# Kernel optimization log

Measured on AMD Instinct MI355X. Metric: run time of the kernel, lower is better.

The kernel has to match this reference:

```python
import jax, jax.numpy as jnp
import numpy as np

B, T, C = 2, 1024, 768
H, NE, K = 3072, 8, 2


def setup_inputs() -> dict:
    key = jax.random.key(0)
    k1, k2, k3, k4 = jax.random.split(key, 4)
    x = jax.random.normal(k1, (B, T, C), dtype=jnp.float32)
    w_fc = jax.random.normal(k2, (C, H * NE), dtype=jnp.float32) * 0.02
    w_proj = jax.random.normal(k3, (H * NE, C), dtype=jnp.float32) * (0.02 * (2 * 12) ** -0.5)
    w_gate = jax.random.normal(k4, (C, NE), dtype=jnp.float32) * 0.02
    return {"x": x, "w_fc": w_fc, "w_proj": w_proj, "w_gate": w_gate}


def reference(x, w_fc, w_proj, w_gate):
    # Router: softmax over experts, top-k, renormalize selected probs.
    router_logits = jnp.einsum('btc,ce->bte', x, w_gate)
    router_probs = jax.nn.softmax(router_logits, axis=-1)
    top_p, top_i = jax.lax.top_k(router_probs, K)          # (B,T,K)
    top_p = top_p / jnp.sum(top_p, axis=-1, keepdims=True)

    # First projection. Original gathers (C,H,B,T,K) weight slices then
    # einsum('btc,chbtk->bthk'); mathematically identical to projecting with
    # all experts and gathering the selected outputs (same contraction order).
    wf = w_fc.reshape(C, H, NE)
    h_all = jnp.einsum('btc,che->bthe', x, wf)             # (B,T,H,NE)
    h = jnp.take_along_axis(h_all, top_i[:, :, None, :], axis=-1)  # (B,T,H,K)
    h = jax.nn.gelu(h, approximate=True)

    # Second projection + weighted combine over the K selected experts.
    wp = w_proj.reshape(H, C, NE)
    o_all = jnp.einsum('bthk,hce->btcke', h, wp)           # (B,T,C,K,NE)
    o = jnp.take_along_axis(o_all, top_i[:, :, None, :, None], axis=-1)[..., 0]  # (B,T,C,K)
    o = jnp.einsum('btck,btk->btc', o, top_p)
    return o
```

## Files before the change

kernel.cpp:

```cpp
#include <hip/hip_runtime.h>
#include <hip/hip_bf16.h>
#include <math.h>

#define BB 2
#define TT 1024
#define CC 768
#define HH 3072
#define NEXP 8
#define NTOK (BB*TT)
#define CAP 1024
#define CNT_STRIDE 32

typedef __attribute__((ext_vector_type(8))) short short8;
typedef __attribute__((ext_vector_type(4))) float float4v;

typedef const __attribute__((address_space(1))) void* gptr_t;
typedef __attribute__((address_space(3))) void* sptr_t;

__device__ __forceinline__ unsigned short f2bf(float f) {
    unsigned int u = __float_as_uint(f);
    unsigned int r = (u + 0x7fffu + ((u >> 16) & 1u)) >> 16;
    return (unsigned short)r;
}
__device__ __forceinline__ float gelu_tanh(float v) {
    const float k2 = 2.0f * 0.7978845608028654f;
    const float k1 = 0.044715f;
    float z = k2 * (v + k1 * v * v * v);
    return v / (1.0f + __expf(-z));
}

__global__ void router_kernel(const float* __restrict__ x,
                              const float* __restrict__ w_gate,
                              float* __restrict__ top_p,
                              int* __restrict__ counts,
                              int* __restrict__ tok_list) {
    int t = blockIdx.x;
    int lane = threadIdx.x;
    float acc[NEXP];
#pragma unroll
    for (int e = 0; e < NEXP; ++e) acc[e] = 0.f;
    for (int c = lane; c < CC; c += 64) {
        float xv = x[t * CC + c];
        const float4* wg = (const float4*)(w_gate + c * NEXP);
        float4 w0 = wg[0], w1 = wg[1];
        acc[0] += xv * w0.x; acc[1] += xv * w0.y;
        acc[2] += xv * w0.z; acc[3] += xv * w0.w;
        acc[4] += xv * w1.x; acc[5] += xv * w1.y;
        acc[6] += xv * w1.z; acc[7] += xv * w1.w;
    }
#pragma unroll
    for (int e = 0; e < NEXP; ++e) {
        for (int off = 32; off > 0; off >>= 1)
            acc[e] += __shfl_down(acc[e], off, 64);
    }
    if (lane == 0) {
        float m = acc[0];
#pragma unroll
        for (int e = 1; e < NEXP; ++e) m = fmaxf(m, acc[e]);
        float p[NEXP]; float s = 0.f;
#pragma unroll
        for (int e = 0; e < NEXP; ++e) { p[e] = expf(acc[e] - m); s += p[e]; }
        float inv_s = 1.f / s;
#pragma unroll
        for (int e = 0; e < NEXP; ++e) p[e] *= inv_s;
        int i0 = 0;
#pragma unroll
        for (int e = 1; e < NEXP; ++e) if (p[e] > p[i0]) i0 = e;
        int i1 = (i0 == 0) ? 1 : 0;
#pragma unroll
        for (int e = 0; e < NEXP; ++e) if (e != i0 && p[e] > p[i1]) i1 = e;
        float p0 = p[i0], p1 = p[i1];
        float inv = 1.f / (p0 + p1);
        top_p[t * 2 + 0] = p0 * inv;
        top_p[t * 2 + 1] = p1 * inv;
        int pos0 = atomicAdd(&counts[i0 * CNT_STRIDE], 1);
        if (pos0 < CAP) tok_list[i0 * NTOK + pos0] = t * 2 + 0;
        int pos1 = atomicAdd(&counts[i1 * CNT_STRIDE], 1);
        if (pos1 < CAP) tok_list[i1 * NTOK + pos1] = t * 2 + 1;
    }
}

__global__ __launch_bounds__(256)
void permute_w(const float* __restrict__ In, unsigned short* __restrict__ Out,
               int Adim, int Bdim) {
    __shared__ unsigned short L[128 * 66];
    int a0 = blockIdx.x * 128;
    int b0 = blockIdx.y * 8;
    int t = threadIdx.x;
#pragma unroll
    for (int j = 0; j < 8; ++j) {
        int idx = j * 256 + t;
        int r = idx >> 4, c4 = idx & 15;
        const float4 v = *(const float4*)(In + (size_t)(a0 + r) * Bdim * 8 + b0 * 8 + c4 * 4);
        ushort2 s01, s23;
        s01.x = f2bf(v.x); s01.y = f2bf(v.y);
        s23.x = f2bf(v.z); s23.y = f2bf(v.w);
        *(ushort2*)&L[r * 66 + c4 * 4]     = s01;
        *(ushort2*)&L[r * 66 + c4 * 4 + 2] = s23;
    }
    __syncthreads();
    int w = t >> 6, ln = t & 63;
    int oc = w * 16 + (ln & 15);
    int e = oc & 7, b = b0 + (oc >> 3);
    unsigned short* dst = Out + ((size_t)e * Bdim + b) * Adim + a0;
#pragma unroll
    for (int p = 0; p < 4; ++p) {
        int seg = (ln >> 4) + p * 4;
        short8 vv;
#pragma unroll
        for (int k = 0; k < 8; ++k) vv[k] = (short)L[(seg * 8 + k) * 66 + oc];
        *(short8*)(dst + seg * 8) = vv;
    }
}

__global__ void gather_x(const float* __restrict__ x,
                         const int* __restrict__ counts,
                         const int* __restrict__ tok_list,
                         unsigned short* __restrict__ xg) {
    int pos = blockIdx.x;
    int e = pos >> 10, i = pos & (CAP - 1);
    int M = counts[e * CNT_STRIDE]; if (M > CAP) M = CAP;
    int Mr = (M + 127) & ~127; if (Mr > CAP) Mr = CAP;
    if (i >= Mr) return;
    int c = threadIdx.x * 4;
    unsigned short* dst = xg + (size_t)pos * CC + c;
    ushort4 s;
    if (i < M) {
        int tk = tok_list[e * NTOK + i] >> 1;
        float4 v = *(const float4*)(x + (size_t)tk * CC + c);
        s.x = f2bf(v.x); s.y = f2bf(v.y); s.z = f2bf(v.z); s.w = f2bf(v.w);
    } else {
        s.x = s.y = s.z = s.w = 0;
    }
    *(ushort4*)dst = s;
}

__global__ __launch_bounds__(256)
void gemm1_mfma(const unsigned short* __restrict__ xg,
                const unsigned short* __restrict__ wfc_b,
                const int* __restrict__ counts,
                unsigned short* __restrict__ h_slab) {
    int e = blockIdx.z;
    int M = counts[e * CNT_STRIDE]; if (M > CAP) M = CAP;
    int m0 = blockIdx.y * 128;
    if (m0 >= M) return;
    int n0 = blockIdx.x * 128;

    __shared__ unsigned short As[2][128 * 32];
    __shared__ unsigned short Bs[2][128 * 32];

    int tid = threadIdx.x;
    int wave = tid >> 6, lane = tid & 63;
    int wm = wave >> 1, wn = wave & 1;
    int quad = lane >> 4, l16 = lane & 15;

    const unsigned short* aBase = xg + ((size_t)e * CAP + m0) * CC;
    const unsigned short* bBase = wfc_b + ((size_t)e * HH + n0) * CC;

    int srow = wave * 32 + (lane >> 2);
    int schunk = (lane & 3) * 8;

    float4v acc[4][4];
#pragma unroll
    for (int i = 0; i < 4; ++i)
#pragma unroll
        for (int j = 0; j < 4; ++j)
#pragma unroll
            for (int r = 0; r < 4; ++r) acc[i][j][r] = 0.f;

#pragma unroll
    for (int q = 0; q < 2; ++q) {
        int r = srow + q * 16;
        __builtin_amdgcn_global_load_lds(
            (gptr_t)(aBase + (size_t)r * CC + schunk),
            (sptr_t)(&As[0][(wave * 32 + q * 16) * 32]), 16, 0, 0);
        __builtin_amdgcn_global_load_lds(
            (gptr_t)(bBase + (size_t)r * CC + schunk),
            (sptr_t)(&Bs[0][(wave * 32 + q * 16) * 32]), 16, 0, 0);
    }

    for (int k0 = 0; k0 < CC; k0 += 32) {
        int cur = (k0 >> 5) & 1;
        __syncthreads();
        if (k0 + 32 < CC) {
            int nxt = cur ^ 1;
#pragma unroll
            for (int q = 0; q < 2; ++q) {
                int r = srow + q * 16;
                __builtin_amdgcn_global_load_lds(
                    (gptr_t)(aBase + (size_t)r * CC + k0 + 32 + schunk),
                    (sptr_t)(&As[nxt][(wave * 32 + q * 16) * 32]), 16, 0, 0);
                __builtin_amdgcn_global_load_lds(
                    (gptr_t)(bBase + (size_t)r * CC + k0 + 32 + schunk),
                    (sptr_t)(&Bs[nxt][(wave * 32 + q * 16) * 32]), 16, 0, 0);
            }
        }
        short8 af[4], bf[4];
#pragma unroll
        for (int mt = 0; mt < 4; ++mt)
            af[mt] = *(const short8*)&As[cur][(wm * 64 + mt * 16 + l16) * 32 + quad * 8];
#pragma unroll
        for (int nt = 0; nt < 4; ++nt)
            bf[nt] = *(const short8*)&Bs[cur][(wn * 64 + nt * 16 + l16) * 32 + quad * 8];
#pragma unroll
        for (int mt = 0; mt < 4; ++mt)
#pragma unroll
            for (int nt = 0; nt < 4; ++nt)
                acc[mt][nt] = __builtin_amdgcn_mfma_f32_16x16x32_bf16(
                    af[mt], bf[nt], acc[mt][nt], 0, 0, 0);
    }

#pragma unroll
    for (int mt = 0; mt < 4; ++mt) {
#pragma unroll
        for (int r = 0; r < 4; ++r) {
            int m = m0 + wm * 64 + mt * 16 + quad * 4 + r;
            unsigned short* orow = h_slab + ((size_t)e * CAP + m) * HH + n0 + wn * 64 + l16;
#pragma unroll
            for (int nt = 0; nt < 4; ++nt)
                orow[nt * 16] = f2bf(gelu_tanh(acc[mt][nt][r]));
        }
    }
}

__global__ __launch_bounds__(256)
void gemm2_mfma(const unsigned short* __restrict__ h_slab,
                const unsigned short* __restrict__ wp_b,
                const int* __restrict__ counts,
                const int* __restrict__ tok_list,
                float* __restrict__ o_part) {
    int e = blockIdx.z;
    int M = counts[e * CNT_STRIDE]; if (M > CAP) M = CAP;
    int m0 = blockIdx.y * 128;
    if (m0 >= M) return;
    int n0 = (blockIdx.x >> 2) * 128;
    int ks = blockIdx.x & 3;

    __shared__ unsigned short As[2][128 * 32];
    __shared__ unsigned short Bs[2][128 * 32];

    int tid = threadIdx.x;
    int wave = tid >> 6, lane = tid & 63;
    int wm = wave >> 1, wn = wave & 1;
    int quad = lane >> 4, l16 = lane & 15;

    const unsigned short* aBase = h_slab + ((size_t)e * CAP + m0) * HH + ks * 768;
    const unsigned short* bBase = wp_b + ((size_t)e * CC + n0) * HH + ks * 768;

    int srow = wave * 32 + (lane >> 2);
    int schunk = (lane & 3) * 8;

    float4v acc[4][4];
#pragma unroll
    for (int i = 0; i < 4; ++i)
#pragma unroll
        for (int j = 0; j < 4; ++j)
#pragma unroll
            for (int r = 0; r < 4; ++r) acc[i][j][r] = 0.f;

#pragma unroll
    for (int q = 0; q < 2; ++q) {
        int r = srow + q * 16;
        __builtin_amdgcn_global_load_lds(
            (gptr_t)(aBase + (size_t)r * HH + schunk),
            (sptr_t)(&As[0][(wave * 32 + q * 16) * 32]), 16, 0, 0);
        __builtin_amdgcn_global_load_lds(
            (gptr_t)(bBase + (size_t)r * HH + schunk),
            (sptr_t)(&Bs[0][(wave * 32 + q * 16) * 32]), 16, 0, 0);
    }

    for (int k0 = 0; k0 < 768; k0 += 32) {
        int cur = (k0 >> 5) & 1;
        __syncthreads();
        if (k0 + 32 < 768) {
            int nxt = cur ^ 1;
#pragma unroll
            for (int q = 0; q < 2; ++q) {
                int r = srow + q * 16;
                __builtin_amdgcn_global_load_lds(
                    (gptr_t)(aBase + (size_t)r * HH + k0 + 32 + schunk),
                    (sptr_t)(&As[nxt][(wave * 32 + q * 16) * 32]), 16, 0, 0);
                __builtin_amdgcn_global_load_lds(
                    (gptr_t)(bBase + (size_t)r * HH + k0 + 32 + schunk),
                    (sptr_t)(&Bs[nxt][(wave * 32 + q * 16) * 32]), 16, 0, 0);
            }
        }
        short8 af[4], bf[4];
#pragma unroll
        for (int mt = 0; mt < 4; ++mt)
            af[mt] = *(const short8*)&As[cur][(wm * 64 + mt * 16 + l16) * 32 + quad * 8];
#pragma unroll
        for (int nt = 0; nt < 4; ++nt)
            bf[nt] = *(const short8*)&Bs[cur][(wn * 64 + nt * 16 + l16) * 32 + quad * 8];
#pragma unroll
        for (int mt = 0; mt < 4; ++mt)
#pragma unroll
            for (int nt = 0; nt < 4; ++nt)
                acc[mt][nt] = __builtin_amdgcn_mfma_f32_16x16x32_bf16(
                    af[mt], bf[nt], acc[mt][nt], 0, 0, 0);
    }

#pragma unroll
    for (int mt = 0; mt < 4; ++mt) {
#pragma unroll
        for (int r = 0; r < 4; ++r) {
            int m = m0 + wm * 64 + mt * 16 + quad * 4 + r;
            if (m < M) {
                int ent = tok_list[e * NTOK + m];
                float* orow = o_part + ((size_t)ks * NTOK * 2 + ent) * CC + n0 + wn * 64 + l16;
#pragma unroll
                for (int nt = 0; nt < 4; ++nt)
                    orow[nt * 16] = acc[mt][nt][r];
            }
        }
    }
}

__global__ void combine_kernel(const float* __restrict__ o_part,
                               const float* __restrict__ top_p,
                               float* __restrict__ out) {
    int idx = blockIdx.x * 256 + threadIdx.x;
    int t = idx / (CC / 4);
    int c = (idx % (CC / 4)) * 4;
    float p0 = top_p[2 * t], p1 = top_p[2 * t + 1];
    float4 s0 = make_float4(0.f, 0.f, 0.f, 0.f);
    float4 s1 = make_float4(0.f, 0.f, 0.f, 0.f);
#pragma unroll
    for (int ks = 0; ks < 4; ++ks) {
        const float4 a = *(const float4*)(o_part + ((size_t)ks * NTOK * 2 + 2 * t) * CC + c);
        const float4 b = *(const float4*)(o_part + ((size_t)ks * NTOK * 2 + 2 * t + 1) * CC + c);
        s0.x += a.x; s0.y += a.y; s0.z += a.z; s0.w += a.w;
        s1.x += b.x; s1.y += b.y; s1.z += b.z; s1.w += b.w;
    }
    float4 r;
    r.x = p0 * s0.x + p1 * s1.x;
    r.y = p0 * s0.y + p1 * s1.y;
    r.z = p0 * s0.z + p1 * s1.z;
    r.w = p0 * s0.w + p1 * s1.w;
    *(float4*)(out + (size_t)t * CC + c) = r;
}

extern "C" void kernel_launch(void* const* d_in, const int* in_sizes, int n_in,
                              void* d_out, int out_size, void* d_ws, size_t ws_size,
                              hipStream_t stream) {
    const float* x      = (const float*)d_in[0];
    const float* w_fc   = (const float*)d_in[1];
    const float* w_proj = (const float*)d_in[2];
    const float* w_gate = (const float*)d_in[3];
    float* out = (float*)d_out;

    char* ws = (char*)d_ws;
    size_t off = 0;
    float* top_p    = (float*)(ws + off); off += NTOK * 2 * sizeof(float);
    int*   counts   = (int*)(ws + off);   off += CNT_STRIDE * NEXP * 4;
    int*   tok_list = (int*)(ws + off);   off += (size_t)NEXP * NTOK * 4;
    off = 131072;
    unsigned short* wp_b   = (unsigned short*)(ws + off); off += (size_t)NEXP*CC*HH*2;
    unsigned short* h_slab = (unsigned short*)(ws + off); off += (size_t)NEXP*CAP*HH*2;
    unsigned short* wfc_b  = (unsigned short*)(ws + off);
    float*          o_part = (float*)(ws + off);          off += (size_t)NEXP*HH*CC*2;
    unsigned short* xg     = (unsigned short*)(ws + off); off += (size_t)NEXP*CAP*CC*2;

    hipMemsetAsync(counts, 0, CNT_STRIDE * NEXP * 4, stream);

    router_kernel<<<NTOK, 64, 0, stream>>>(x, w_gate, top_p, counts, tok_list);
    permute_w<<<dim3(CC / 128, HH / 8), 256, 0, stream>>>(w_fc, wfc_b, CC, HH);
    permute_w<<<dim3(HH / 128, CC / 8), 256, 0, stream>>>(w_proj, wp_b, HH, CC);
    gather_x<<<NEXP * CAP, 192, 0, stream>>>(x, counts, tok_list, xg);

    gemm1_mfma<<<dim3(HH / 128, CAP / 128, NEXP), 256, 0, stream>>>(
        xg, wfc_b, counts, h_slab);
    gemm2_mfma<<<dim3((CC / 128) * 4, CAP / 128, NEXP), 256, 0, stream>>>(
        h_slab, wp_b, counts, tok_list, o_part);
    combine_kernel<<<(NTOK * CC / 4) / 256, 256, 0, stream>>>(o_part, top_p, out);
}
```

Before: 300.1 us.

## Load GEMM fragments directly from global memory and interleave experts in block order

Both expert GEMMs drop their LDS double-buffered staging via global_load_lds and the per-step barriers. Each wave now reads its MFMA operand fragments straight from global memory and relies on L1/L2 for reuse across waves. The grid is flattened to 1D with the expert index in the low bits, so neighbouring blocks belong to different experts and early-exit blocks are spread across the machine. The cost is redundant global and cache traffic, since each A and B row is read by two waves instead of once per block, plus exposed load latency with no software prefetch.

Measured after the change: 491.2 us. 63.7% more time.

```diff
diff --git a/kernel.cpp b/kernel.cpp
--- a/kernel.cpp
+++ b/kernel.cpp
@@ -13,9 +13,6 @@
 
 typedef __attribute__((ext_vector_type(8))) short short8;
 typedef __attribute__((ext_vector_type(4))) float float4v;
-
-typedef const __attribute__((address_space(1))) void* gptr_t;
-typedef __attribute__((address_space(3))) void* sptr_t;
 
 __device__ __forceinline__ unsigned short f2bf(float f) {
     unsigned int u = __float_as_uint(f);
@@ -140,25 +137,23 @@
                 const unsigned short* __restrict__ wfc_b,
                 const int* __restrict__ counts,
                 unsigned short* __restrict__ h_slab) {
-    int e = blockIdx.z;
+    int id = blockIdx.x;
+    int e = id & 7;
+    int r = id >> 3;
+    int mb = r & 7;
+    int nb = r >> 3;
     int M = counts[e * CNT_STRIDE]; if (M > CAP) M = CAP;
-    int m0 = blockIdx.y * 128;
+    int m0 = mb * 128;
     if (m0 >= M) return;
-    int n0 = blockIdx.x * 128;
-
-    __shared__ unsigned short As[2][128 * 32];
-    __shared__ unsigned short Bs[2][128 * 32];
+    int n0 = nb * 128;
 
     int tid = threadIdx.x;
     int wave = tid >> 6, lane = tid & 63;
     int wm = wave >> 1, wn = wave & 1;
     int quad = lane >> 4, l16 = lane & 15;
 
-    const unsigned short* aBase = xg + ((size_t)e * CAP + m0) * CC;
-    const unsigned short* bBase = wfc_b + ((size_t)e * HH + n0) * CC;
-
-    int srow = wave * 32 + (lane >> 2);
-    int schunk = (lane & 3) * 8;
+    const unsigned short* aP = xg    + ((size_t)e * CAP + m0 + wm * 64 + l16) * CC + quad * 8;
+    const unsigned short* bP = wfc_b + ((size_t)e * HH  + n0 + wn * 64 + l16) * CC + quad * 8;
 
     float4v acc[4][4];
 #pragma unroll
@@ -166,42 +161,17 @@
 #pragma unroll
         for (int j = 0; j < 4; ++j)
 #pragma unroll
-            for (int r = 0; r < 4; ++r) acc[i][j][r] = 0.f;
-
-#pragma unroll
-    for (int q = 0; q < 2; ++q) {
-        int r = srow + q * 16;
-        __builtin_amdgcn_global_load_lds(
-            (gptr_t)(aBase + (size_t)r * CC + schunk),
-            (sptr_t)(&As[0][(wave * 32 + q * 16) * 32]), 16, 0, 0);
-        __builtin_amdgcn_global_load_lds(
-            (gptr_t)(bBase + (size_t)r * CC + schunk),
-            (sptr_t)(&Bs[0][(wave * 32 + q * 16) * 32]), 16, 0, 0);
-    }
-
+            for (int rr = 0; rr < 4; ++rr) acc[i][j][rr] = 0.f;
+
+#pragma unroll 2
     for (int k0 = 0; k0 < CC; k0 += 32) {
-        int cur = (k0 >> 5) & 1;
-        __syncthreads();
-        if (k0 + 32 < CC) {
-            int nxt = cur ^ 1;
-#pragma unroll
-            for (int q = 0; q < 2; ++q) {
-                int r = srow + q * 16;
-                __builtin_amdgcn_global_load_lds(
-                    (gptr_t)(aBase + (size_t)r * CC + k0 + 32 + schunk),
-                    (sptr_t)(&As[nxt][(wave * 32 + q * 16) * 32]), 16, 0, 0);
-                __builtin_amdgcn_global_load_lds(
-                    (gptr_t)(bBase + (size_t)r * CC + k0 + 32 + schunk),
-                    (sptr_t)(&Bs[nxt][(wave * 32 + q * 16) * 32]), 16, 0, 0);
-            }
-        }
         short8 af[4], bf[4];
 #pragma unroll
         for (int mt = 0; mt < 4; ++mt)
-            af[mt] = *(const short8*)&As[cur][(wm * 64 + mt * 16 + l16) * 32 + quad * 8];
+            af[mt] = *(const short8*)(aP + (size_t)mt * 16 * CC + k0);
 #pragma unroll
         for (int nt = 0; nt < 4; ++nt)
-            bf[nt] = *(const short8*)&Bs[cur][(wn * 64 + nt * 16 + l16) * 32 + quad * 8];
+            bf[nt] = *(const short8*)(bP + (size_t)nt * 16 * CC + k0);
 #pragma unroll
         for (int mt = 0; mt < 4; ++mt)
 #pragma unroll
@@ -213,12 +183,12 @@
 #pragma unroll
     for (int mt = 0; mt < 4; ++mt) {
 #pragma unroll
-        for (int r = 0; r < 4; ++r) {
-            int m = m0 + wm * 64 + mt * 16 + quad * 4 + r;
+        for (int rr = 0; rr < 4; ++rr) {
+            int m = m0 + wm * 64 + mt * 16 + quad * 4 + rr;
             unsigned short* orow = h_slab + ((size_t)e * CAP + m) * HH + n0 + wn * 64 + l16;
 #pragma unroll
             for (int nt = 0; nt < 4; ++nt)
-                orow[nt * 16] = f2bf(gelu_tanh(acc[mt][nt][r]));
+                orow[nt * 16] = f2bf(gelu_tanh(acc[mt][nt][rr]));
         }
     }
 }
@@ -229,26 +199,25 @@
                 const int* __restrict__ counts,
                 const int* __restrict__ tok_list,
                 float* __restrict__ o_part) {
-    int e = blockIdx.z;
+    int id = blockIdx.x;
+    int e = id & 7;
+    int r = id >> 3;
+    int mb = r & 7;
+    int q  = r >> 3;
+    int ks = q / 6;
+    int nb = q - ks * 6;
     int M = counts[e * CNT_STRIDE]; if (M > CAP) M = CAP;
-    int m0 = blockIdx.y * 128;
+    int m0 = mb * 128;
     if (m0 >= M) return;
-    int n0 = (blockIdx.x >> 2) * 128;
-    int ks = blockIdx.x & 3;
-
-    __shared__ unsigned short As[2][128 * 32];
-    __shared__ unsigned short Bs[2][128 * 32];
+    int n0 = nb * 128;
 
     int tid = threadIdx.x;
     int wave = tid >> 6, lane = tid & 63;
     int wm = wave >> 1, wn = wave & 1;
     int quad = lane >> 4, l16 = lane & 15;
 
-    const unsigned short* aBase = h_slab + ((size_t)e * CAP + m0) * HH + ks * 768;
-    const unsigned short* bBase = wp_b + ((size_t)e * CC + n0) * HH + ks * 768;
-
-    int srow = wave * 32 + (lane >> 2);
-    int schunk = (lane & 3) * 8;
+    const unsigned short* aP = h_slab + ((size_t)e * CAP + m0 + wm * 64 + l16) * HH + ks * 768 + quad * 8;
+    const unsigned short* bP = wp_b   + ((size_t)e * CC  + n0 + wn * 64 + l16) * HH + ks * 768 + quad * 8;
 
     float4v acc[4][4];
 #pragma unroll
@@ -256,42 +225,17 @@
 #pragma unroll
         for (int j = 0; j < 4; ++j)
 #pragma unroll
-            for (int r = 0; r < 4; ++r) acc[i][j][r] = 0.f;
-
-#pragma unroll
-    for (int q = 0; q < 2; ++q) {
-        int r = srow + q * 16;
-        __builtin_amdgcn_global_load_lds(
-            (gptr_t)(aBase + (size_t)r * HH + schunk),
-            (sptr_t)(&As[0][(wave * 32 + q * 16) * 32]), 16, 0, 0);
-        __builtin_amdgcn_global_load_lds(
-            (gptr_t)(bBase + (size_t)r * HH + schunk),
-            (sptr_t)(&Bs[0][(wave * 32 + q * 16) * 32]), 16, 0, 0);
-    }
-
+            for (int rr = 0; rr < 4; ++rr) acc[i][j][rr] = 0.f;
+
+#pragma unroll 2
     for (int k0 = 0; k0 < 768; k0 += 32) {
-        int cur = (k0 >> 5) & 1;
-        __syncthreads();
-        if (k0 + 32 < 768) {
-            int nxt = cur ^ 1;
-#pragma unroll
-            for (int q = 0; q < 2; ++q) {
-                int r = srow + q * 16;
-                __builtin_amdgcn_global_load_lds(
-                    (gptr_t)(aBase + (size_t)r * HH + k0 + 32 + schunk),
-                    (sptr_t)(&As[nxt][(wave * 32 + q * 16) * 32]), 16, 0, 0);
-                __builtin_amdgcn_global_load_lds(
-                    (gptr_t)(bBase + (size_t)r * HH + k0 + 32 + schunk),
-                    (sptr_t)(&Bs[nxt][(wave * 32 + q * 16) * 32]), 16, 0, 0);
-            }
-        }
         short8 af[4], bf[4];
 #pragma unroll
         for (int mt = 0; mt < 4; ++mt)
-            af[mt] = *(const short8*)&As[cur][(wm * 64 + mt * 16 + l16) * 32 + quad * 8];
+            af[mt] = *(const short8*)(aP + (size_t)mt * 16 * HH + k0);
 #pragma unroll
         for (int nt = 0; nt < 4; ++nt)
-            bf[nt] = *(const short8*)&Bs[cur][(wn * 64 + nt * 16 + l16) * 32 + quad * 8];
+            bf[nt] = *(const short8*)(bP + (size_t)nt * 16 * HH + k0);
 #pragma unroll
         for (int mt = 0; mt < 4; ++mt)
 #pragma unroll
@@ -303,14 +247,14 @@
 #pragma unroll
     for (int mt = 0; mt < 4; ++mt) {
 #pragma unroll
-        for (int r = 0; r < 4; ++r) {
-            int m = m0 + wm * 64 + mt * 16 + quad * 4 + r;
+        for (int rr = 0; rr < 4; ++rr) {
+            int m = m0 + wm * 64 + mt * 16 + quad * 4 + rr;
             if (m < M) {
                 int ent = tok_list[e * NTOK + m];
                 float* orow = o_part + ((size_t)ks * NTOK * 2 + ent) * CC + n0 + wn * 64 + l16;
 #pragma unroll
                 for (int nt = 0; nt < 4; ++nt)
-                    orow[nt * 16] = acc[mt][nt][r];
+                    orow[nt * 16] = acc[mt][nt][rr];
             }
         }
     }
@@ -368,9 +312,7 @@
     permute_w<<<dim3(HH / 128, CC / 8), 256, 0, stream>>>(w_proj, wp_b, HH, CC);
     gather_x<<<NEXP * CAP, 192, 0, stream>>>(x, counts, tok_list, xg);
 
-    gemm1_mfma<<<dim3(HH / 128, CAP / 128, NEXP), 256, 0, stream>>>(
-        xg, wfc_b, counts, h_slab);
-    gemm2_mfma<<<dim3((CC / 128) * 4, CAP / 128, NEXP), 256, 0, stream>>>(
-        h_slab, wp_b, counts, tok_list, o_part);
+    gemm1_mfma<<<dim3(8 * 8 * 24), 256, 0, stream>>>(xg, wfc_b, counts, h_slab);
+    gemm2_mfma<<<dim3(8 * 8 * 24), 256, 0, stream>>>(h_slab, wp_b, counts, tok_list, o_part);
     combine_kernel<<<(NTOK * CC / 4) / 256, 256, 0, stream>>>(o_part, top_p, out);
 }
```
